# Optimization experiments

Hardware: AMD Instinct MI355X
Metric: run time of the kernel (lower is better)

## Reference

```python
import jax, jax.numpy as jnp
import numpy as np

N, E = 50000, 800000
F_IN, HID, HEADS = 128, 32, 8
H1 = HID * HEADS            # 256: conv1 concat output, also conv2 in/out
NUM_WALKS, WALK_LEN = 512, 64
WINDOW, NEG_S = 5, 10
TEMP = 0.07
NEG_SLOPE = 0.2


def setup_inputs() -> dict:
    key = jax.random.key(0)
    ks = jax.random.split(key, 16)
    inp = {
        "x": jax.random.normal(ks[0], (N, F_IN), jnp.float32),
        "edge_index": jax.random.randint(ks[1], (2, E), 0, N),
        "walks": jax.random.randint(ks[2], (NUM_WALKS, WALK_LEN), 0, N),
        "neg_nodes": jax.random.randint(ks[3], (NUM_WALKS, WALK_LEN, NEG_S), 0, N),
        # conv1 params (GATConv: in=F_IN, out=HID, heads=HEADS, concat)
        "W1": jax.random.normal(ks[4], (F_IN, HEADS * HID), jnp.float32) / np.sqrt(F_IN),
        "a_src1": jax.random.normal(ks[5], (HEADS, HID), jnp.float32) / np.sqrt(HID),
        "a_dst1": jax.random.normal(ks[6], (HEADS, HID), jnp.float32) / np.sqrt(HID),
        "b1": jnp.zeros((HEADS * HID,), jnp.float32),
        # conv2 params (GATConv: in=H1, out=H1, heads=1)
        "W2": jax.random.normal(ks[7], (H1, H1), jnp.float32) / np.sqrt(H1),
        "a_src2": jax.random.normal(ks[8], (1, H1), jnp.float32) / np.sqrt(H1),
        "a_dst2": jax.random.normal(ks[9], (1, H1), jnp.float32) / np.sqrt(H1),
        "b2": jnp.zeros((H1,), jnp.float32),
    }
    return inp


def gat_conv(x, edge_index, W, a_src, a_dst, b, heads, out_ch):
    """PyG-style GATConv: self-loops, per-dst softmax attention, concat heads."""
    n = x.shape[0]
    loops = jnp.arange(n)
    src = jnp.concatenate([edge_index[0], loops])
    dst = jnp.concatenate([edge_index[1], loops])
    xw = (x @ W).reshape(n, heads, out_ch)                  # [N,H,C]
    al_s = jnp.einsum('nhc,hc->nh', xw, a_src)              # [N,H]
    al_d = jnp.einsum('nhc,hc->nh', xw, a_dst)
    e = jax.nn.leaky_relu(al_s[src] + al_d[dst], NEG_SLOPE)  # [Et,H]
    m = jax.ops.segment_max(e, dst, num_segments=n)
    ex = jnp.exp(e - m[dst])
    den = jax.ops.segment_sum(ex, dst, num_segments=n)
    alpha = ex / den[dst]                                    # [Et,H]
    out = jax.ops.segment_sum(alpha[:, :, None] * xw[src], dst, num_segments=n)
    return out.reshape(n, heads * out_ch) + b


def walk_contrastive_loss(emb, walks, neg_nodes):
    eps = 1e-8
    nrm = emb / jnp.clip(jnp.linalg.norm(emb, axis=-1, keepdims=True), eps)
    L = walks.shape[1]
    offs = jnp.concatenate([jnp.arange(-WINDOW, 0), jnp.arange(1, WINDOW + 1)])  # [2W]
    pos_pos = jnp.arange(L)[:, None] + offs[None, :]        # [L,2W]
    pos_valid = (pos_pos >= 0) & (pos_pos < L)
    pos_nodes = walks[:, jnp.clip(pos_pos, 0, L - 1)]       # [B,L,2W]
    anchor = nrm[walks]                                      # [B,L,D]
    pos_sims = jnp.einsum('bld,blpd->blp', anchor, nrm[pos_nodes]) / TEMP
    neg_sims = jnp.einsum('bld,blsd->bls', anchor, nrm[neg_nodes]) / TEMP
    # drop negatives that collide with (valid) positives, as torch.isin filter does
    neg_in_pos = ((neg_nodes[:, :, :, None] == pos_nodes[:, :, None, :])
                  & pos_valid[None, :, None, :]).any(-1)     # [B,L,S]
    pos_sum = jnp.sum(jnp.exp(pos_sims) * pos_valid[None].astype(emb.dtype), axis=-1)
    neg_sum = jnp.sum(jnp.exp(neg_sims) * (~neg_in_pos).astype(emb.dtype), axis=-1)
    has_pos = pos_valid.any(-1)[None]                        # [1,L]
    safe_pos = jnp.where(has_pos, pos_sum, 1.0)
    term = -jnp.log(safe_pos / (safe_pos + neg_sum))
    return jnp.sum(jnp.where(has_pos, term, 0.0))


def reference(x, edge_index, walks, neg_nodes, W1, a_src1, a_dst1, b1,
              W2, a_src2, a_dst2, b2):
    emb1 = jax.nn.elu(gat_conv(x, edge_index, W1, a_src1, a_dst1, b1, HEADS, HID))
    emb2 = gat_conv(emb1, edge_index, W2, a_src2, a_dst2, b2, 1, H1)
    emb = jnp.concatenate([emb1, emb2], axis=1)              # [N, 2*H1]
    return walk_contrastive_loss(emb, walks, neg_nodes)
```

## Files before the change

### kernel.cpp

```cpp
#include <hip/hip_runtime.h>
#include <math.h>

#define N_NODES 50000
#define N_PAD 50048
#define E_EDGES 800000
#define E_PAD (E_EDGES + 8 * N_NODES)
#define FDIM_IN 128
#define HID_1 32
#define HEADS_1 8
#define H1DIM 256
#define NUM_WALKS 512
#define WALK_LEN 64
#define WINDOW 5
#define NEG_S 10
#define TEMP 0.07f
#define INV_TEMP (1.0f / 0.07f)
#define NEG_SLOPE 0.2f
#define LOG2E 1.44269504f

#define SCAN_BLOCKS ((N_NODES + 255) / 256)

#define NB 98
#define GCAP 12288
#define LCAP 64
#define BIN_BLOCKS 392
#define WINCAP 16384

typedef unsigned int uint;
typedef unsigned short ushort;
typedef long long i64_t;
typedef __attribute__((ext_vector_type(8))) short bf16x8;
typedef __attribute__((ext_vector_type(8))) ushort us8;
typedef __attribute__((ext_vector_type(4))) float f32x4;
typedef __attribute__((ext_vector_type(2))) float vf2;
typedef __attribute__((ext_vector_type(2))) i64_t i64x2;
typedef __attribute__((ext_vector_type(4))) uint u32x4;

__device__ __forceinline__ float leaky(float v) {
    return fmaxf(v, v * NEG_SLOPE);
}

__device__ __forceinline__ float bfl(uint u) { return __uint_as_float(u << 16); }
__device__ __forceinline__ float bfh(uint u) { return __uint_as_float(u & 0xffff0000u); }

__device__ __forceinline__ ushort f2bf(float x) {
    uint u = __float_as_uint(x);
    u = u + 0x7fffu + ((u >> 16) & 1u);
    return (ushort)(u >> 16);
}

__device__ __forceinline__ uint pk4fp8(float a, float b, float c, float d) {
    int u = __builtin_amdgcn_cvt_pk_fp8_f32(a, b, 0, false);
    u = __builtin_amdgcn_cvt_pk_fp8_f32(c, d, u, true);
    return (uint)u;
}

__device__ __forceinline__ float red16(float x) {
    int v = __float_as_int(x);
    x += __int_as_float(__builtin_amdgcn_update_dpp(0, v, 0xB1, 0xF, 0xF, true));
    v = __float_as_int(x);
    x += __int_as_float(__builtin_amdgcn_update_dpp(0, v, 0x4E, 0xF, 0xF, true));
    v = __float_as_int(x);
    x += __int_as_float(__builtin_amdgcn_update_dpp(0, v, 0x141, 0xF, 0xF, true));
    v = __float_as_int(x);
    x += __int_as_float(__builtin_amdgcn_update_dpp(0, v, 0x140, 0xF, 0xF, true));
    return x;
}


#define PB_CVT  6250
#define PO_WT1  (PB_CVT)
#define PO_WT2  (PO_WT1 + 128)
#define PO_MISC (PO_WT2 + 256)
#define PREP_GRID (PO_MISC + 1)

__global__ __launch_bounds__(256) void prep_kernel(
        const float* __restrict__ x,
        const float* __restrict__ W1, const float* __restrict__ W2,
        uint* __restrict__ xb, ushort* __restrict__ wt1, ushort* __restrict__ wt2,
        float* __restrict__ als1, float* __restrict__ als2, uint* __restrict__ xw8) {
    const int blk = blockIdx.x, t = threadIdx.x;
    if (blk < PB_CVT) {
        int i = blk * 256 + t;
        float4 v = ((const float4*)x)[i];
        uint2 p;
        p.x = (uint)f2bf(v.x) | ((uint)f2bf(v.y) << 16);
        p.y = (uint)f2bf(v.z) | ((uint)f2bf(v.w) << 16);
        ((uint2*)xb)[i] = p;
    } else if (blk < PO_WT2) {
        int tid = (blk - PO_WT1) * 256 + t;
        int k = tid >> 8, n = tid & 255;
        wt1[n * 128 + k] = f2bf(W1[k * 256 + n]);
    } else if (blk < PO_MISC) {
        int tid = (blk - PO_WT2) * 256 + t;
        int k = tid >> 8, n = tid & 255;
        wt2[n * 256 + k] = f2bf(W2[k * 256 + n]);
    } else {
        if (t < HEADS_1) als1[N_NODES * HEADS_1 + t] = -1e30f;
        if (t == HEADS_1) als2[N_NODES] = -1e30f;
        if (t >= 64 && t < 128) xw8[N_NODES * 64 + (t - 64)] = 0u;
    }
}


__global__ __launch_bounds__(256) void bin_kernel(
        const int* __restrict__ ei, int* __restrict__ deg,
        uint* __restrict__ gbucket, int* __restrict__ gcur) {
    __shared__ int scnt[NB];
    __shared__ int gposs[NB];
    __shared__ uint sbuf[NB * LCAP];
    const int t = threadIdx.x;
    if (t < NB) scnt[t] = 0;
    __syncthreads();
    const int e0 = blockIdx.x * 2048;
#pragma unroll
    for (int k = 0; k < 8; k++) {
        int e = e0 + k * 256 + t;
        if (e < E_EDGES) {
            int dst = ei[E_EDGES + e];
            int src = ei[e];
            atomicAdd(&deg[dst], 1);
            uint packed = ((uint)dst << 16) | (uint)src;
            int bk = dst >> 9;
            int pos = atomicAdd(&scnt[bk], 1);
            if (pos < LCAP) sbuf[bk * LCAP + pos] = packed;
            else {
                int gp = atomicAdd(&gcur[bk], 1);
                gbucket[bk * GCAP + gp] = packed;
            }
        }
    }
    __syncthreads();
    if (t < NB) {
        int c = scnt[t]; if (c > LCAP) c = LCAP;
        gposs[t] = atomicAdd(&gcur[t], c);
        scnt[t] = c;
    }
    __syncthreads();
    const int w = t >> 6, lane = t & 63;
    for (int b = w; b < NB; b += 4) {
        int c = scnt[b], gp = gposs[b];
        for (int i = lane; i < c; i += 64)
            gbucket[b * GCAP + gp + i] = sbuf[b * LCAP + i];
    }
}


__global__ __launch_bounds__(256) void scan_a(const int* __restrict__ deg,
                                              int* __restrict__ excl,
                                              int* __restrict__ bsum) {
    __shared__ int s[256];
    int t = threadIdx.x;
    int i = blockIdx.x * 256 + t;
    int d = (i < N_NODES) ? deg[i] : 0;
    int v = (d + 7) & ~7;
    s[t] = v;
    __syncthreads();
    for (int off = 1; off < 256; off <<= 1) {
        int tmp = (t >= off) ? s[t - off] : 0;
        __syncthreads();
        s[t] += tmp;
        __syncthreads();
    }
    if (i < N_NODES) excl[i] = s[t] - v;
    if (t == 255) bsum[blockIdx.x] = s[255];
}

__global__ __launch_bounds__(256) void scan_b(int* __restrict__ bsum) {
    __shared__ int s[256];
    int t = threadIdx.x;
    int v = (t < SCAN_BLOCKS) ? bsum[t] : 0;
    s[t] = v;
    __syncthreads();
    for (int off = 1; off < 256; off <<= 1) {
        int tmp = (t >= off) ? s[t - off] : 0;
        __syncthreads();
        s[t] += tmp;
        __syncthreads();
    }
    if (t < SCAN_BLOCKS) bsum[t] = s[t] - v;
}

__global__ void scan_c2(const int* __restrict__ deg,
                        int* __restrict__ excl, const int* __restrict__ bsum,
                        int* __restrict__ row_start) {
    int i = blockIdx.x * blockDim.x + threadIdx.x;
    if (i < N_NODES) {
        int rs = excl[i] + bsum[i >> 8];
        row_start[i] = rs;
        if (i == N_NODES - 1) row_start[N_NODES] = rs + ((deg[i] + 7) & ~7);
    }
}


__global__ __launch_bounds__(256) void scatter_kernel(
        const uint* __restrict__ gbucket, const int* __restrict__ gcur,
        const int* __restrict__ row_start, ushort* __restrict__ srclist) {
    __shared__ ushort win[WINCAP];
    __shared__ int cur[512];
    const int b = blockIdx.x, t = threadIdx.x;
    const int nlo = b << 9;
    const int nhi = (nlo + 512 < N_NODES) ? (nlo + 512) : N_NODES;
    const int base = row_start[nlo];
    const int end = row_start[nhi];
    const int span = end - base;
    for (int i = t; i < nhi - nlo; i += 256) cur[i] = row_start[nlo + i] - base;
    for (int i = t; i < span / 2; i += 256) ((uint*)win)[i] = 0xC350C350u;
    __syncthreads();
    const int cnt = gcur[b];
    for (int i = t; i < cnt; i += 256) {
        uint packed = gbucket[b * GCAP + i];
        int dst = packed >> 16;
        int slot = atomicAdd(&cur[dst - nlo], 1);
        win[slot] = (ushort)(packed & 0xffffu);
    }
    __syncthreads();
    u32x4* d4 = (u32x4*)(srclist + base);
    const u32x4* s4 = (const u32x4*)win;
    for (int i = t; i < span / 8; i += 256) d4[i] = s4[i];
}

template<int K, int H>
__global__ __launch_bounds__(256) void mfma_gemm64(
        const ushort* __restrict__ A,
        const ushort* __restrict__ Wt,
        uint* __restrict__ Y8,
        const float* __restrict__ a_src,
        const float* __restrict__ a_dst,
        float* __restrict__ als, float* __restrict__ ald) {
    constexpr int KP = K + 8;
    constexpr int K8 = K / 8;
    __shared__ __align__(16) ushort As[64 * KP];
    __shared__ float sals[64][5], sald[64][5];
    const int m0 = blockIdx.x * 64;
    const int t = threadIdx.x;
    const uint4* Ag = (const uint4*)(A + (size_t)m0 * K);
    uint4* As4 = (uint4*)As;
    for (int i = t; i < 64 * K8; i += 256) {
        int r = i / K8, c8 = i % K8;
        As4[r * (K8 + 1) + c8] = Ag[i];
    }
    __syncthreads();
    const int wv = __builtin_amdgcn_readfirstlane(t >> 6);
    const int lane = t & 63;
    const int n0 = wv * 64;
    const int mrow = lane & 15, q = lane >> 4;
    f32x4 acc[4][4];
#pragma unroll
    for (int mt = 0; mt < 4; mt++)
#pragma unroll
        for (int i = 0; i < 4; i++) acc[mt][i] = (f32x4){0.f, 0.f, 0.f, 0.f};
#pragma unroll
    for (int k0 = 0; k0 < K; k0 += 32) {
        bf16x8 a[4], b[4];
#pragma unroll
        for (int mt = 0; mt < 4; mt++)
            a[mt] = *(const bf16x8*)(As + (mt * 16 + mrow) * KP + k0 + q * 8);
#pragma unroll
        for (int i = 0; i < 4; i++)
            b[i] = *(const bf16x8*)(Wt + (uint)(n0 + i * 16 + mrow) * K + k0 + q * 8);
#pragma unroll
        for (int mt = 0; mt < 4; mt++)
#pragma unroll
            for (int i = 0; i < 4; i++)
                acc[mt][i] = __builtin_amdgcn_mfma_f32_16x16x32_bf16(a[mt], b[i], acc[mt][i], 0, 0, 0);
    }
    {
        float as[4], ad[4];
#pragma unroll
        for (int i = 0; i < 4; i++) {
            as[i] = a_src[n0 + i * 16 + mrow];
            ad[i] = a_dst[n0 + i * 16 + mrow];
        }
#pragma unroll
        for (int mt = 0; mt < 4; mt++) {
#pragma unroll
            for (int r = 0; r < 4; r++) {
                const int row = m0 + mt * 16 + q * 4 + r;
                if (H == 8) {
                    float ps0 = acc[mt][0][r] * as[0] + acc[mt][1][r] * as[1];
                    float ps1 = acc[mt][2][r] * as[2] + acc[mt][3][r] * as[3];
                    float pd0 = acc[mt][0][r] * ad[0] + acc[mt][1][r] * ad[1];
                    float pd1 = acc[mt][2][r] * ad[2] + acc[mt][3][r] * ad[3];
#pragma unroll
                    for (int o = 1; o < 16; o <<= 1) {
                        ps0 += __shfl_xor(ps0, o, 64); ps1 += __shfl_xor(ps1, o, 64);
                        pd0 += __shfl_xor(pd0, o, 64); pd1 += __shfl_xor(pd1, o, 64);
                    }
                    if (mrow == 0 && row < N_NODES) {
                        als[row * 8 + 2 * wv] = ps0 * LOG2E;
                        als[row * 8 + 2 * wv + 1] = ps1 * LOG2E;
                        ald[row * 8 + 2 * wv] = pd0 * LOG2E;
                        ald[row * 8 + 2 * wv + 1] = pd1 * LOG2E;
                    }
                } else {
                    float ps = acc[mt][0][r] * as[0] + acc[mt][1][r] * as[1]
                             + acc[mt][2][r] * as[2] + acc[mt][3][r] * as[3];
                    float pd = acc[mt][0][r] * ad[0] + acc[mt][1][r] * ad[1]
                             + acc[mt][2][r] * ad[2] + acc[mt][3][r] * ad[3];
#pragma unroll
                    for (int o = 1; o < 16; o <<= 1) {
                        ps += __shfl_xor(ps, o, 64); pd += __shfl_xor(pd, o, 64);
                    }
                    if (mrow == 0) {
                        sals[mt * 16 + q * 4 + r][wv] = ps;
                        sald[mt * 16 + q * 4 + r][wv] = pd;
                    }
                }
            }
        }
    }
    __syncthreads();
    if (H == 1 && t < 64) {
        const int row = m0 + t;
        if (row < N_NODES) {
            als[row] = (sals[t][0] + sals[t][1] + sals[t][2] + sals[t][3]) * LOG2E;
            ald[row] = (sald[t][0] + sald[t][1] + sald[t][2] + sald[t][3]) * LOG2E;
        }
    }
    float* S = (float*)As + wv * 16 * 68;
    const int prow = lane >> 2, pj = lane & 3;
#pragma unroll
    for (int mt = 0; mt < 4; mt++) {
#pragma unroll
        for (int i = 0; i < 4; i++)
#pragma unroll
            for (int r = 0; r < 4; r++)
                S[(q * 4 + r) * 68 + i * 16 + mrow] = acc[mt][i][r];
        const float* cp = S + prow * 68 + pj * 16;
        uint4 o;
        o.x = pk4fp8(cp[0],  cp[1],  cp[2],  cp[3]);
        o.y = pk4fp8(cp[4],  cp[5],  cp[6],  cp[7]);
        o.z = pk4fp8(cp[8],  cp[9],  cp[10], cp[11]);
        o.w = pk4fp8(cp[12], cp[13], cp[14], cp[15]);
        const int row = m0 + mt * 16 + prow;
        if (row < N_NODES)
            ((uint4*)(Y8 + (size_t)row * 64))[wv * 4 + pj] = o;
    }
}

__global__ __launch_bounds__(256) void gat_gather1(
        const int* __restrict__ row_start, const ushort* __restrict__ srclist,
        const float* __restrict__ als, const float* __restrict__ ald,
        const uint* __restrict__ xw8,
        const float* __restrict__ bias,
        ushort* __restrict__ emb1b) {
    const int wid = __builtin_amdgcn_readfirstlane(blockIdx.x * 4 + (threadIdx.x >> 6));
    const uint lane = threadIdx.x & 63;
    const uint h = lane >> 3;
    const float ald_n = ald[wid * HEADS_1 + h];
    const int beg = row_start[wid], end = row_start[wid + 1];

    float ex0 = __builtin_amdgcn_exp2f(leaky(als[wid * HEADS_1 + h] + ald_n));
    uint u = xw8[((uint)wid << 6) + lane];
    vf2 lo = __builtin_amdgcn_cvt_pk_f32_fp8((int)u, false);
    vf2 hi = __builtin_amdgcn_cvt_pk_f32_fp8((int)u, true);
    float den = ex0;
    vf2 exv0 = {ex0, ex0};
    vf2 a01 = exv0 * lo, a23 = exv0 * hi;

    for (int i = beg; i < end; i += 8) {
        us8 sv = *(const us8*)(srclist + i);
        uint rr[8]; float ee[8];
#pragma unroll
        for (int j = 0; j < 8; j++) rr[j] = xw8[((uint)sv[j] << 6) + lane];
#pragma unroll
        for (int j = 0; j < 8; j++) ee[j] = als[(uint)sv[j] * HEADS_1 + h];
#pragma unroll
        for (int j = 0; j < 8; j++) {
            float ex = __builtin_amdgcn_exp2f(leaky(ee[j] + ald_n));
            vf2 l2 = __builtin_amdgcn_cvt_pk_f32_fp8((int)rr[j], false);
            vf2 h2 = __builtin_amdgcn_cvt_pk_f32_fp8((int)rr[j], true);
            den += ex;
            vf2 exv = {ex, ex};
            a01 += exv * l2;
            a23 += exv * h2;
        }
    }
    float inv = 1.f / den;
    float4 bv = ((const float4*)bias)[lane];
    float4 r;
    r.x = a01[0] * inv + bv.x; r.y = a01[1] * inv + bv.y;
    r.z = a23[0] * inv + bv.z; r.w = a23[1] * inv + bv.w;
    r.x = r.x > 0.f ? r.x : __expf(r.x) - 1.f;
    r.y = r.y > 0.f ? r.y : __expf(r.y) - 1.f;
    r.z = r.z > 0.f ? r.z : __expf(r.z) - 1.f;
    r.w = r.w > 0.f ? r.w : __expf(r.w) - 1.f;
    uint2 p;
    p.x = (uint)f2bf(r.x) | ((uint)f2bf(r.y) << 16);
    p.y = (uint)f2bf(r.z) | ((uint)f2bf(r.w) << 16);
    ((uint2*)emb1b)[((uint)wid << 6) + lane] = p;
}

__global__ __launch_bounds__(256) void gat_gather2(
        const int* __restrict__ row_start, const ushort* __restrict__ srclist,
        const float* __restrict__ als, const float* __restrict__ ald,
        const uint* __restrict__ xw8,
        const float* __restrict__ bias,
        const ushort* __restrict__ emb1b,
        uint* __restrict__ embn8) {
    const int wid = __builtin_amdgcn_readfirstlane(blockIdx.x * 4 + (threadIdx.x >> 6));
    const uint lane = threadIdx.x & 63;
    const float ald_n = ald[wid];
    const int beg = row_start[wid], end = row_start[wid + 1];

    float ex0 = __builtin_amdgcn_exp2f(leaky(als[wid] + ald_n));
    uint u = xw8[((uint)wid << 6) + lane];
    vf2 lo = __builtin_amdgcn_cvt_pk_f32_fp8((int)u, false);
    vf2 hi = __builtin_amdgcn_cvt_pk_f32_fp8((int)u, true);
    float den = ex0;
    vf2 exv0 = {ex0, ex0};
    vf2 a01 = exv0 * lo, a23 = exv0 * hi;

    for (int i = beg; i < end; i += 8) {
        us8 sv = *(const us8*)(srclist + i);
        uint rr[8]; float ee[8];
#pragma unroll
        for (int j = 0; j < 8; j++) rr[j] = xw8[((uint)sv[j] << 6) + lane];
#pragma unroll
        for (int j = 0; j < 8; j++) ee[j] = als[(uint)sv[j]];
#pragma unroll
        for (int j = 0; j < 8; j++) {
            float ex = __builtin_amdgcn_exp2f(leaky(ee[j] + ald_n));
            vf2 l2 = __builtin_amdgcn_cvt_pk_f32_fp8((int)rr[j], false);
            vf2 h2 = __builtin_amdgcn_cvt_pk_f32_fp8((int)rr[j], true);
            den += ex;
            vf2 exv = {ex, ex};
            a01 += exv * l2;
            a23 += exv * h2;
        }
    }
    float inv = 1.f / den;
    float4 bv = ((const float4*)bias)[lane];
    float4 e2;
    e2.x = a01[0] * inv + bv.x; e2.y = a01[1] * inv + bv.y;
    e2.z = a23[0] * inv + bv.z; e2.w = a23[1] * inv + bv.w;
    uint2 u1 = ((const uint2*)emb1b)[((uint)wid << 6) + lane];
    float4 e1;
    e1.x = bfl(u1.x); e1.y = bfh(u1.x); e1.z = bfl(u1.y); e1.w = bfh(u1.y);

    float ssum = e1.x * e1.x + e1.y * e1.y + e1.z * e1.z + e1.w * e1.w
               + e2.x * e2.x + e2.y * e2.y + e2.z * e2.z + e2.w * e2.w;
#pragma unroll
    for (int o = 32; o > 0; o >>= 1) ssum += __shfl_xor(ssum, o, 64);
    float innv = 1.f / fmaxf(sqrtf(ssum), 1e-8f);

    uint p1 = pk4fp8(e1.x * innv, e1.y * innv, e1.z * innv, e1.w * innv);
    uint p2 = pk4fp8(e2.x * innv, e2.y * innv, e2.z * innv, e2.w * innv);
    const uint n1 = ((lane >> 4) << 4) | (((lane >> 1) & 3) << 2) | (((lane >> 3) & 1) << 1) | (lane & 1);
    embn8[((uint)wid << 7) + n1] = p1;
    embn8[((uint)wid << 7) + 64 + n1] = p2;
}


#define ROWU 140

__global__ __launch_bounds__(1024, 8) void loss_mfma_kernel(
        const uint* __restrict__ embn8,
        const int* __restrict__ walks, const int* __restrict__ negs,
        float* __restrict__ out) {
    __shared__ __align__(16) uint srows8[WALK_LEN * ROWU];
    __shared__ int wids[WALK_LEN];
    __shared__ float possum[WALK_LEN];
    __shared__ float negsum[WALK_LEN];
    const int b = blockIdx.x;
    const int t = threadIdx.x;
    const int w = __builtin_amdgcn_readfirstlane(t >> 6);
    const int lane = t & 63;
    const int mrow = lane & 15, q = lane >> 4;
    const char* embc = (const char*)embn8;

    if (t < 64) wids[t] = walks[b * WALK_LEN + t];
    else if (t < 128) possum[t - 64] = 0.f;
    else if (t < 192) negsum[t - 128] = 0.f;

    uint4 Bv[8];
    int pnode = negs[b * (WALK_LEN * NEG_S) + (w * 16 + mrow)];
    {
        const char* bp = embc + (((uint)pnode) << 9) + (uint)(q * 16);
#pragma unroll
        for (int j = 0; j < 8; j++) Bv[j] = *(const uint4*)(bp + j * 64);
    }
    __syncthreads();

    {
        const int rA = w * 4 + (lane >> 5);
        const int rB = rA + 2;
        const uint off = lane & 31;
        ((uint4*)(srows8 + rA * ROWU))[off] = ((const uint4*)embn8)[((uint)wids[rA] << 5) + off];
        ((uint4*)(srows8 + rB * ROWU))[off] = ((const uint4*)embn8)[((uint)wids[rB] << 5) + off];
    }
    __syncthreads();

#pragma unroll
    for (int ji = 0; ji < 3; ji++) {
        const int job = w + ji * 16;
        f32x4 acc0 = {0.f, 0.f, 0.f, 0.f};
        f32x4 acc1 = {0.f, 0.f, 0.f, 0.f};
        if (ji < 2 || w < 8) {
            const int albase = (job / 10) * 16;
            const int curnode = pnode;
            const int owner = (job * 16 + mrow) / 10;
            const char* ap = (const char*)(srows8 + (albase + mrow) * ROWU) + q * 16;
            __builtin_amdgcn_s_setprio(1);
#pragma unroll
            for (int j = 0; j < 4; j++) {
                i64x2 a = *(const i64x2*)(ap + j * 64);
                const i64x2 bb = *(const i64x2*)&Bv[j];
                acc0 = __builtin_amdgcn_mfma_f32_16x16x32_fp8_fp8(a[0], bb[0], acc0, 0, 0, 0);
                acc0 = __builtin_amdgcn_mfma_f32_16x16x32_fp8_fp8(a[1], bb[1], acc0, 0, 0, 0);
            }
#pragma unroll
            for (int j = 4; j < 8; j++) {
                i64x2 a = *(const i64x2*)(ap + j * 64);
                const i64x2 bb = *(const i64x2*)&Bv[j];
                acc1 = __builtin_amdgcn_mfma_f32_16x16x32_fp8_fp8(a[0], bb[0], acc1, 0, 0, 0);
                acc1 = __builtin_amdgcn_mfma_f32_16x16x32_fp8_fp8(a[1], bb[1], acc1, 0, 0, 0);
            }
            __builtin_amdgcn_s_setprio(0);
            if (ji == 0 || (ji == 1 && w < 8)) {
                const int njob = job + 16;
                pnode = negs[b * (WALK_LEN * NEG_S) + (njob * 16 + mrow)];
                const char* bp = embc + (((uint)pnode) << 9) + (uint)(q * 16);
#pragma unroll
                for (int j = 0; j < 8; j++) Bv[j] = *(const uint4*)(bp + j * 64);
            }
#pragma unroll
            for (int reg = 0; reg < 4; reg++) {
                const int l_a = albase + q * 4 + reg;
                float e = 0.f;
                if (owner == l_a) {
                    bool msk = false;
#pragma unroll
                    for (int dj = -WINDOW; dj <= WINDOW; dj++) {
                        if (dj == 0) continue;
                        int p = l_a + dj;
                        if (p >= 0 && p < WALK_LEN && wids[p] == curnode) msk = true;
                    }
                    if (!msk) e = __expf((acc0[reg] + acc1[reg]) * INV_TEMP);
                }
                e = red16(e);
                if (mrow == 0 && e != 0.f) atomicAdd(&negsum[l_a], e);
            }
        } else {
            const int pj = w - 8;
            const int g = pj >> 1, half = pj & 1;
            const int albase = g * 16;
            const int base = (albase - WINDOW) > 0 ? (albase - WINDOW) : 0;
            const int hi = (albase + 15 + WINDOW) < (WALK_LEN - 1) ? (albase + 15 + WINDOW) : (WALK_LEN - 1);
            const int cnt = hi - base + 1;
            const int r = half * 16 + mrow;
            const int row = base + r;
            const int rc = row < hi ? row : hi;
            const char* ap = (const char*)(srows8 + (albase + mrow) * ROWU) + q * 16;
            const char* bp = (const char*)(srows8 + rc * ROWU) + q * 16;
            __builtin_amdgcn_s_setprio(1);
#pragma unroll
            for (int j = 0; j < 4; j++) {
                i64x2 a = *(const i64x2*)(ap + j * 64);
                i64x2 bb = *(const i64x2*)(bp + j * 64);
                acc0 = __builtin_amdgcn_mfma_f32_16x16x32_fp8_fp8(a[0], bb[0], acc0, 0, 0, 0);
                acc0 = __builtin_amdgcn_mfma_f32_16x16x32_fp8_fp8(a[1], bb[1], acc0, 0, 0, 0);
            }
#pragma unroll
            for (int j = 4; j < 8; j++) {
                i64x2 a = *(const i64x2*)(ap + j * 64);
                i64x2 bb = *(const i64x2*)(bp + j * 64);
                acc1 = __builtin_amdgcn_mfma_f32_16x16x32_fp8_fp8(a[0], bb[0], acc1, 0, 0, 0);
                acc1 = __builtin_amdgcn_mfma_f32_16x16x32_fp8_fp8(a[1], bb[1], acc1, 0, 0, 0);
            }
            __builtin_amdgcn_s_setprio(0);
#pragma unroll
            for (int reg = 0; reg < 4; reg++) {
                const int l_a = albase + q * 4 + reg;
                const int d = row - l_a;
                bool use = (r < cnt) && (d != 0) && (d >= -WINDOW) && (d <= WINDOW);
                float e = use ? __expf((acc0[reg] + acc1[reg]) * INV_TEMP) : 0.f;
                e = red16(e);
                if (mrow == 0 && e != 0.f) atomicAdd(&possum[l_a], e);
            }
        }
    }
    __syncthreads();
    if (t < 64) {
        float term = logf(1.f + negsum[t] / possum[t]);
#pragma unroll
        for (int o = 32; o > 0; o >>= 1) term += __shfl_xor(term, o, 64);
        if (t == 0) atomicAdd(out, term);
    }
}

extern "C" void kernel_launch(void* const* d_in, const int* in_sizes, int n_in,
                              void* d_out, int out_size, void* d_ws, size_t ws_size,
                              hipStream_t stream) {
    const float* x      = (const float*)d_in[0];
    const int*   ei     = (const int*)d_in[1];
    const int*   walks  = (const int*)d_in[2];
    const int*   negs   = (const int*)d_in[3];
    const float* W1     = (const float*)d_in[4];
    const float* a_src1 = (const float*)d_in[5];
    const float* a_dst1 = (const float*)d_in[6];
    const float* b1     = (const float*)d_in[7];
    const float* W2     = (const float*)d_in[8];
    const float* a_src2 = (const float*)d_in[9];
    const float* a_dst2 = (const float*)d_in[10];
    const float* b2     = (const float*)d_in[11];
    float* out = (float*)d_out;

    float* ws = (float*)d_ws;
    size_t off = 0;
#define ALIGN_OFF off = (off + 255) & ~(size_t)255
    float* r_xw8   = ws + off; off += (size_t)(N_NODES + 1) * 64;  ALIGN_OFF;
    float* r_emb1b = ws + off; off += (size_t)N_PAD * 128;         ALIGN_OFF;
    float* r_embn8 = ws + off; off += (size_t)N_NODES * 128;       ALIGN_OFF;
    float* r_xb    = ws + off; off += (size_t)N_PAD * 64;          ALIGN_OFF;
    float* r_wt1   = ws + off; off += 256 * 64;                    ALIGN_OFF;
    float* r_wt2   = ws + off; off += 256 * 128;                   ALIGN_OFF;
    float* als1  = ws + off; off += (N_NODES + 1) * HEADS_1;       ALIGN_OFF;
    float* ald1  = ws + off; off += N_NODES * HEADS_1;             ALIGN_OFF;
    float* als2  = ws + off; off += N_NODES + 1;                   ALIGN_OFF;
    float* ald2  = ws + off; off += N_NODES;                       ALIGN_OFF;
    int* deg       = (int*)(ws + off); off += N_NODES;             ALIGN_OFF;
    int* excl      = (int*)(ws + off); off += N_NODES;             ALIGN_OFF;
    int* bsum      = (int*)(ws + off); off += 256;                 ALIGN_OFF;
    int* row_start = (int*)(ws + off); off += N_NODES + 1;         ALIGN_OFF;
    uint* gbucket  = (uint*)(ws + off); off += (size_t)NB * GCAP;  ALIGN_OFF;
    int* gcur      = (int*)(ws + off); off += 256;                 ALIGN_OFF;
    ushort* srclist = (ushort*)(ws + off); off += E_PAD / 2;       ALIGN_OFF;
    uint*   xw8   = (uint*)r_xw8;
    ushort* emb1b = (ushort*)r_emb1b;
    uint*   embn8 = (uint*)r_embn8;
    ushort* xb    = (ushort*)r_xb;
    ushort* wt1   = (ushort*)r_wt1;
    ushort* wt2   = (ushort*)r_wt2;

    hipMemsetAsync(out, 0, sizeof(float) * out_size, stream);
    hipMemsetAsync(deg, 0, sizeof(int) * N_NODES, stream);
    hipMemsetAsync(gcur, 0, sizeof(int) * NB, stream);

    prep_kernel<<<PREP_GRID, 256, 0, stream>>>(
        x, W1, W2, (uint*)xb, wt1, wt2, als1, als2, xw8);

    bin_kernel<<<BIN_BLOCKS, 256, 0, stream>>>(ei, deg, gbucket, gcur);

    scan_a<<<SCAN_BLOCKS, 256, 0, stream>>>(deg, excl, bsum);
    scan_b<<<1, 256, 0, stream>>>(bsum);
    scan_c2<<<SCAN_BLOCKS, 256, 0, stream>>>(deg, excl, bsum, row_start);

    scatter_kernel<<<NB, 256, 0, stream>>>(gbucket, gcur, row_start, srclist);

    mfma_gemm64<128, HEADS_1><<<N_PAD / 64, 256, 0, stream>>>(
        xb, wt1, xw8, a_src1, a_dst1, als1, ald1);
    gat_gather1<<<N_NODES / 4, 256, 0, stream>>>(
        row_start, srclist, als1, ald1, xw8, b1, emb1b);

    mfma_gemm64<256, 1><<<N_PAD / 64, 256, 0, stream>>>(
        emb1b, wt2, xw8, a_src2, a_dst2, als2, ald2);
    gat_gather2<<<N_NODES / 4, 256, 0, stream>>>(
        row_start, srclist, als2, ald2, xw8, b2, emb1b, embn8);

    loss_mfma_kernel<<<NUM_WALKS, 1024, 0, stream>>>(embn8, walks, negs, out);
}
```

Measured before the change: 335.4 us.

## Fuse edge binning into prep kernel and CSR scatter into first GEMM launch

Edge binning moves into the prep kernel as extra blocks, and the CSR scatter runs as leading blocks of the first GEMM launch, so two kernel launches go away and independent work overlaps. Degree counters and global buckets are replicated across 8 groups to cut atomic contention, and the scan sums the per-group degrees. The costs are larger memsets, more degree reads in the scan, and scatter blocks that now walk 8 bucket groups. The GEMM shared memory is also enlarged to hold the scatter window, which may lower occupancy.

```diff
diff --git a/kernel.cpp b/kernel.cpp
--- a/kernel.cpp
+++ b/kernel.cpp
@@ -21,10 +21,10 @@
 #define SCAN_BLOCKS ((N_NODES + 255) / 256)
 
 #define NB 98
-#define GCAP 12288
-#define LCAP 64
-#define BIN_BLOCKS 392
-#define WINCAP 16384
+#define NGRP 8
+#define GCAP 1536
+#define LCAP 32
+#define BIN_BLOCKS 784
 
 typedef unsigned int uint;
 typedef unsigned short ushort;
@@ -72,12 +72,14 @@
 #define PO_WT1  (PB_CVT)
 #define PO_WT2  (PO_WT1 + 128)
 #define PO_MISC (PO_WT2 + 256)
-#define PREP_GRID (PO_MISC + 1)
+#define PO_BIN  (PO_MISC + 1)
+#define PREP_GRID (PO_BIN + BIN_BLOCKS)
 
 __global__ __launch_bounds__(256) void prep_kernel(
-        const float* __restrict__ x,
+        const float* __restrict__ x, const int* __restrict__ ei,
         const float* __restrict__ W1, const float* __restrict__ W2,
         uint* __restrict__ xb, ushort* __restrict__ wt1, ushort* __restrict__ wt2,
+        int* __restrict__ degp, uint* __restrict__ gbucket, int* __restrict__ gcur,
         float* __restrict__ als1, float* __restrict__ als2, uint* __restrict__ xw8) {
     const int blk = blockIdx.x, t = threadIdx.x;
     if (blk < PB_CVT) {
@@ -95,64 +97,66 @@
         int tid = (blk - PO_WT2) * 256 + t;
         int k = tid >> 8, n = tid & 255;
         wt2[n * 256 + k] = f2bf(W2[k * 256 + n]);
-    } else {
+    } else if (blk < PO_BIN) {
         if (t < HEADS_1) als1[N_NODES * HEADS_1 + t] = -1e30f;
         if (t == HEADS_1) als2[N_NODES] = -1e30f;
         if (t >= 64 && t < 128) xw8[N_NODES * 64 + (t - 64)] = 0u;
-    }
-}
-
-
-__global__ __launch_bounds__(256) void bin_kernel(
-        const int* __restrict__ ei, int* __restrict__ deg,
-        uint* __restrict__ gbucket, int* __restrict__ gcur) {
-    __shared__ int scnt[NB];
-    __shared__ int gposs[NB];
-    __shared__ uint sbuf[NB * LCAP];
-    const int t = threadIdx.x;
-    if (t < NB) scnt[t] = 0;
-    __syncthreads();
-    const int e0 = blockIdx.x * 2048;
-#pragma unroll
-    for (int k = 0; k < 8; k++) {
-        int e = e0 + k * 256 + t;
-        if (e < E_EDGES) {
-            int dst = ei[E_EDGES + e];
-            int src = ei[e];
-            atomicAdd(&deg[dst], 1);
-            uint packed = ((uint)dst << 16) | (uint)src;
-            int bk = dst >> 9;
-            int pos = atomicAdd(&scnt[bk], 1);
-            if (pos < LCAP) sbuf[bk * LCAP + pos] = packed;
-            else {
-                int gp = atomicAdd(&gcur[bk], 1);
-                gbucket[bk * GCAP + gp] = packed;
-            }
-        }
-    }
-    __syncthreads();
-    if (t < NB) {
-        int c = scnt[t]; if (c > LCAP) c = LCAP;
-        gposs[t] = atomicAdd(&gcur[t], c);
-        scnt[t] = c;
-    }
-    __syncthreads();
-    const int w = t >> 6, lane = t & 63;
-    for (int b = w; b < NB; b += 4) {
-        int c = scnt[b], gp = gposs[b];
-        for (int i = lane; i < c; i += 64)
-            gbucket[b * GCAP + gp + i] = sbuf[b * LCAP + i];
-    }
-}
-
-
-__global__ __launch_bounds__(256) void scan_a(const int* __restrict__ deg,
+    } else {
+        __shared__ int scnt[NB];
+        __shared__ int gposs[NB];
+        __shared__ uint sbuf[NB * LCAP];
+        const int g = blk & 7;
+        int* dg = degp + g * N_NODES;
+        int* gc = gcur + g * NB;
+        uint* gb = gbucket + (size_t)g * NB * GCAP;
+        if (t < NB) scnt[t] = 0;
+        __syncthreads();
+        const int e0 = (blk - PO_BIN) * 1024;
+#pragma unroll
+        for (int k = 0; k < 4; k++) {
+            int e = e0 + k * 256 + t;
+            if (e < E_EDGES) {
+                int dst = ei[E_EDGES + e];
+                int src = ei[e];
+                atomicAdd(&dg[dst], 1);
+                uint packed = ((uint)dst << 16) | (uint)src;
+                int bk = dst >> 9;
+                int pos = atomicAdd(&scnt[bk], 1);
+                if (pos < LCAP) sbuf[bk * LCAP + pos] = packed;
+                else {
+                    int gp = atomicAdd(&gc[bk], 1);
+                    gb[bk * GCAP + gp] = packed;
+                }
+            }
+        }
+        __syncthreads();
+        if (t < NB) {
+            int c = scnt[t]; if (c > LCAP) c = LCAP;
+            gposs[t] = atomicAdd(&gc[t], c);
+            scnt[t] = c;
+        }
+        __syncthreads();
+        const int w2 = t >> 6, lane = t & 63;
+        for (int b2 = w2; b2 < NB; b2 += 4) {
+            int c = scnt[b2], gp = gposs[b2];
+            for (int i = lane; i < c; i += 64)
+                gb[b2 * GCAP + gp + i] = sbuf[b2 * LCAP + i];
+        }
+    }
+}
+
+
+__global__ __launch_bounds__(256) void scan_a(const int* __restrict__ degp,
                                               int* __restrict__ excl,
                                               int* __restrict__ bsum) {
     __shared__ int s[256];
     int t = threadIdx.x;
     int i = blockIdx.x * 256 + t;
-    int d = (i < N_NODES) ? deg[i] : 0;
+    int d = 0;
+    if (i < N_NODES) {
+#pragma unroll
+        for (int g = 0; g < NGRP; g++) d += degp[g * N_NODES + i];
+    }
     int v = (d + 7) & ~7;
     s[t] = v;
     __syncthreads();
@@ -181,43 +185,20 @@
     if (t < SCAN_BLOCKS) bsum[t] = s[t] - v;
 }
 
-__global__ void scan_c2(const int* __restrict__ deg,
+__global__ void scan_c2(const int* __restrict__ degp,
                         int* __restrict__ excl, const int* __restrict__ bsum,
                         int* __restrict__ row_start) {
     int i = blockIdx.x * blockDim.x + threadIdx.x;
     if (i < N_NODES) {
         int rs = excl[i] + bsum[i >> 8];
         row_start[i] = rs;
-        if (i == N_NODES - 1) row_start[N_NODES] = rs + ((deg[i] + 7) & ~7);
-    }
-}
-
-
-__global__ __launch_bounds__(256) void scatter_kernel(
-        const uint* __restrict__ gbucket, const int* __restrict__ gcur,
-        const int* __restrict__ row_start, ushort* __restrict__ srclist) {
-    __shared__ ushort win[WINCAP];
-    __shared__ int cur[512];
-    const int b = blockIdx.x, t = threadIdx.x;
-    const int nlo = b << 9;
-    const int nhi = (nlo + 512 < N_NODES) ? (nlo + 512) : N_NODES;
-    const int base = row_start[nlo];
-    const int end = row_start[nhi];
-    const int span = end - base;
-    for (int i = t; i < nhi - nlo; i += 256) cur[i] = row_start[nlo + i] - base;
-    for (int i = t; i < span / 2; i += 256) ((uint*)win)[i] = 0xC350C350u;
-    __syncthreads();
-    const int cnt = gcur[b];
-    for (int i = t; i < cnt; i += 256) {
-        uint packed = gbucket[b * GCAP + i];
-        int dst = packed >> 16;
-        int slot = atomicAdd(&cur[dst - nlo], 1);
-        win[slot] = (ushort)(packed & 0xffffu);
-    }
-    __syncthreads();
-    u32x4* d4 = (u32x4*)(srclist + base);
-    const u32x4* s4 = (const u32x4*)win;
-    for (int i = t; i < span / 8; i += 256) d4[i] = s4[i];
+        if (i == N_NODES - 1) {
+            int d = 0;
+#pragma unroll
+            for (int g = 0; g < NGRP; g++) d += degp[g * N_NODES + i];
+            row_start[N_NODES] = rs + ((d + 7) & ~7);
+        }
+    }
 }
 
 template<int K, int H>
@@ -227,12 +208,51 @@
         uint* __restrict__ Y8,
         const float* __restrict__ a_src,
         const float* __restrict__ a_dst,
-        float* __restrict__ als, float* __restrict__ ald) {
+        float* __restrict__ als, float* __restrict__ ald,
+        const uint* __restrict__ gbucket, const int* __restrict__ gcur,
+        const int* __restrict__ row_start, ushort* __restrict__ srclist) {
     constexpr int KP = K + 8;
     constexpr int K8 = K / 8;
-    __shared__ __align__(16) ushort As[64 * KP];
-    __shared__ float sals[64][5], sald[64][5];
-    const int m0 = blockIdx.x * 64;
+    constexpr int AS_BYTES = 64 * KP * 2;
+    constexpr int SMEM_BYTES = (H == 8) ? 34816 : (AS_BYTES + 2560);
+    __shared__ __align__(16) char smem[SMEM_BYTES];
+    int m0;
+    if (H == 8) {
+        if (blockIdx.x < NB) {
+            ushort* win = (ushort*)smem;
+            int* cur = (int*)(smem + 32768);
+            const int b = blockIdx.x, t = threadIdx.x;
+            const int nlo = b << 9;
+            const int nhi = (nlo + 512 < N_NODES) ? (nlo + 512) : N_NODES;
+            const int base = row_start[nlo];
+            const int end = row_start[nhi];
+            const int span = end - base;
+            for (int i = t; i < nhi - nlo; i += 256) cur[i] = row_start[nlo + i] - base;
+            for (int i = t; i < span / 2; i += 256) ((uint*)win)[i] = 0xC350C350u;
+            __syncthreads();
+            for (int g = 0; g < NGRP; g++) {
+                const uint* gb = gbucket + ((size_t)g * NB + b) * GCAP;
+                const int cnt = gcur[g * NB + b];
+                for (int i = t; i < cnt; i += 256) {
+                    uint packed = gb[i];
+                    int dst = packed >> 16;
+                    int slot = atomicAdd(&cur[dst - nlo], 1);
+                    win[slot] = (ushort)(packed & 0xffffu);
+                }
+            }
+            __syncthreads();
+            u32x4* d4 = (u32x4*)(srclist + base);
+            const u32x4* s4 = (const u32x4*)win;
+            for (int i = t; i < span / 8; i += 256) d4[i] = s4[i];
+            return;
+        }
+        m0 = (blockIdx.x - NB) * 64;
+    } else {
+        m0 = blockIdx.x * 64;
+    }
+    ushort* As = (ushort*)smem;
+    float (*sals)[5] = (float(*)[5])(smem + AS_BYTES);
+    float (*sald)[5] = (float(*)[5])(smem + AS_BYTES + 1280);
     const int t = threadIdx.x;
     const uint4* Ag = (const uint4*)(A + (size_t)m0 * K);
     uint4* As4 = (uint4*)As;
@@ -318,7 +338,7 @@
             ald[row] = (sald[t][0] + sald[t][1] + sald[t][2] + sald[t][3]) * LOG2E;
         }
     }
-    float* S = (float*)As + wv * 16 * 68;
+    float* S = (float*)smem + wv * 16 * 68;
     const int prow = lane >> 2, pj = lane & 3;
 #pragma unroll
     for (int mt = 0; mt < 4; mt++) {
@@ -620,12 +640,12 @@
     float* ald1  = ws + off; off += N_NODES * HEADS_1;             ALIGN_OFF;
     float* als2  = ws + off; off += N_NODES + 1;                   ALIGN_OFF;
     float* ald2  = ws + off; off += N_NODES;                       ALIGN_OFF;
-    int* deg       = (int*)(ws + off); off += N_NODES;             ALIGN_OFF;
+    int* degp      = (int*)(ws + off); off += (size_t)NGRP * N_NODES; ALIGN_OFF;
     int* excl      = (int*)(ws + off); off += N_NODES;             ALIGN_OFF;
     int* bsum      = (int*)(ws + off); off += 256;                 ALIGN_OFF;
     int* row_start = (int*)(ws + off); off += N_NODES + 1;         ALIGN_OFF;
-    uint* gbucket  = (uint*)(ws + off); off += (size_t)NB * GCAP;  ALIGN_OFF;
-    int* gcur      = (int*)(ws + off); off += 256;                 ALIGN_OFF;
+    uint* gbucket  = (uint*)(ws + off); off += (size_t)NGRP * NB * GCAP; ALIGN_OFF;
+    int* gcur      = (int*)(ws + off); off += 1024;                ALIGN_OFF;
     ushort* srclist = (ushort*)(ws + off); off += E_PAD / 2;       ALIGN_OFF;
     uint*   xw8   = (uint*)r_xw8;
     ushort* emb1b = (ushort*)r_emb1b;
@@ -635,27 +655,23 @@
     ushort* wt2   = (ushort*)r_wt2;
 
     hipMemsetAsync(out, 0, sizeof(float) * out_size, stream);
-    hipMemsetAsync(deg, 0, sizeof(int) * N_NODES, stream);
-    hipMemsetAsync(gcur, 0, sizeof(int) * NB, stream);
+    hipMemsetAsync(degp, 0, sizeof(int) * NGRP * N_NODES, stream);
+    hipMemsetAsync(gcur, 0, sizeof(int) * NGRP * NB, stream);
 
     prep_kernel<<<PREP_GRID, 256, 0, stream>>>(
-        x, W1, W2, (uint*)xb, wt1, wt2, als1, als2, xw8);
-
-    bin_kernel<<<BIN_BLOCKS, 256, 0, stream>>>(ei, deg, gbucket, gcur);
-
-    scan_a<<<SCAN_BLOCKS, 256, 0, stream>>>(deg, excl, bsum);
+        x, ei, W1, W2, (uint*)xb, wt1, wt2, degp, gbucket, gcur, als1, als2, xw8);
+
+    scan_a<<<SCAN_BLOCKS, 256, 0, stream>>>(degp, excl, bsum);
     scan_b<<<1, 256, 0, stream>>>(bsum);
-    scan_c2<<<SCAN_BLOCKS, 256, 0, stream>>>(deg, excl, bsum, row_start);
-
-    scatter_kernel<<<NB, 256, 0, stream>>>(gbucket, gcur, row_start, srclist);
-
-    mfma_gemm64<128, HEADS_1><<<N_PAD / 64, 256, 0, stream>>>(
-        xb, wt1, xw8, a_src1, a_dst1, als1, ald1);
+    scan_c2<<<SCAN_BLOCKS, 256, 0, stream>>>(degp, excl, bsum, row_start);
+
+    mfma_gemm64<128, HEADS_1><<<NB + N_PAD / 64, 256, 0, stream>>>(
+        xb, wt1, xw8, a_src1, a_dst1, als1, ald1, gbucket, gcur, row_start, srclist);
     gat_gather1<<<N_NODES / 4, 256, 0, stream>>>(
         row_start, srclist, als1, ald1, xw8, b1, emb1b);
 
     mfma_gemm64<256, 1><<<N_PAD / 64, 256, 0, stream>>>(
-        emb1b, wt2, xw8, a_src2, a_dst2, als2, ald2);
+        emb1b, wt2, xw8, a_src2, a_dst2, als2, ald2, gbucket, gcur, row_start, srclist);
     gat_gather2<<<N_NODES / 4, 256, 0, stream>>>(
         row_start, srclist, als2, ald2, xw8, b2, emb1b, embn8);
 
```

New measurement: 316.6 us. 5.6% less time.
